# Optimization experiments

Hardware: AMD Instinct MI355X
Metric: run time of the kernel (lower is better)

Reference implementation:

```python
import jax, jax.numpy as jnp
import numpy as np

D_MODEL = 1024
NUM_HEADS = 16
DIM_HEAD = 64
B, NQ, NKV = 2, 2048, 2048


def setup_inputs() -> dict:
    key = jax.random.key(0)
    ks = jax.random.split(key, 12)
    inner = NUM_HEADS * DIM_HEAD
    s_in = 1.0 / np.sqrt(D_MODEL)
    s_o = 1.0 / np.sqrt(inner)
    return {
        "Q": jax.random.normal(ks[0], (B, NQ, D_MODEL), jnp.float32),
        "K": jax.random.normal(ks[1], (B, NKV, D_MODEL), jnp.float32),
        "V": jax.random.normal(ks[2], (B, NKV, D_MODEL), jnp.float32),
        "mask": jax.random.randint(ks[3], (B, 1, NQ, NKV), 0, 2, jnp.int32),
        "W_q": jax.random.normal(ks[4], (D_MODEL, inner), jnp.float32) * s_in,
        "b_q": jnp.zeros((inner,), jnp.float32),
        "W_k": jax.random.normal(ks[5], (D_MODEL, inner), jnp.float32) * s_in,
        "b_k": jnp.zeros((inner,), jnp.float32),
        "W_v": jax.random.normal(ks[6], (D_MODEL, inner), jnp.float32) * s_in,
        "b_v": jnp.zeros((inner,), jnp.float32),
        "W_o": jax.random.normal(ks[7], (inner, D_MODEL), jnp.float32) * s_o,
        "b_o": jnp.zeros((D_MODEL,), jnp.float32),
    }


def reference(Q, K, V, mask, W_q, b_q, W_k, b_k, W_v, b_v, W_o, b_o):
    h, d = NUM_HEADS, DIM_HEAD
    # projections: [b, n, h*d] -> [b, h, n, d]
    def split_heads(x):
        b, n, _ = x.shape
        return x.reshape(b, n, h, d).transpose(0, 2, 1, 3)

    q = split_heads(Q @ W_q + b_q)
    k = split_heads(K @ W_k + b_k)
    v = split_heads(V @ W_v + b_v)

    scores = jnp.einsum("bhqd,bhkd->bhqk", q, k) / jnp.sqrt(jnp.float32(d))
    scores = jnp.where(mask == 0, jnp.float32(-1e9), scores)
    probs = jax.nn.softmax(scores, axis=-1)
    out = jnp.einsum("bhqk,bhkd->bhqd", probs, v)
    out = out.transpose(0, 2, 1, 3).reshape(Q.shape[0], Q.shape[1], h * d)
    return out @ W_o + b_o
```

## Files before the change

### kernel.cpp

```cpp
#include <hip/hip_runtime.h>
#include <hip/hip_bf16.h>
#include <stdint.h>

#define DM   1024
#define NH   16
#define DHD  64
#define BB   2
#define NQS  2048
#define NKVS 2048

typedef __attribute__((ext_vector_type(8))) short short8;
typedef __attribute__((ext_vector_type(4))) float f32x4;
typedef __attribute__((ext_vector_type(16))) float f32x16;
typedef __attribute__((ext_vector_type(4))) unsigned short us4;

static __device__ __forceinline__ unsigned short f2bf(float f) {
  union { float f; unsigned u; } v; v.f = f;
  unsigned r = (v.u + 0x7fffu + ((v.u >> 16) & 1u)) >> 16;
  return (unsigned short)r;
}

#define MFMA(a, b, c)   __builtin_amdgcn_mfma_f32_16x16x32_bf16((a), (b), (c), 0, 0, 0)
#define MFMA32(a, b, c) __builtin_amdgcn_mfma_f32_32x32x16_bf16((a), (b), (c), 0, 0, 0)

__global__ __launch_bounds__(256) void wt_kernel(
    const float* __restrict__ Wq, const float* __restrict__ Wk,
    const float* __restrict__ Wv, const float* __restrict__ Wo,
    unsigned short* __restrict__ wt) {
  __shared__ unsigned short Ls[64][68];
  const int z = blockIdx.z;
  const float* W = (z == 0) ? Wq : (z == 1) ? Wk : (z == 2) ? Wv : Wo;
  unsigned short* out = wt + (size_t)z * 1024 * 1024;
  const int r0 = blockIdx.y * 64, c0 = blockIdx.x * 64;
  const int t = threadIdx.x;
#pragma unroll
  for (int i = 0; i < 4; i++) {
    int idx = t + 256 * i;
    int row = idx >> 4, c4 = (idx & 15) * 4;
    float4 v = *(const float4*)(W + (size_t)(r0 + row) * 1024 + c0 + c4);
    Ls[row][c4 + 0] = f2bf(v.x);
    Ls[row][c4 + 1] = f2bf(v.y);
    Ls[row][c4 + 2] = f2bf(v.z);
    Ls[row][c4 + 3] = f2bf(v.w);
  }
  __syncthreads();
#pragma unroll
  for (int i = 0; i < 4; i++) {
    int idx = t + 256 * i;
    int jj = idx >> 4, k4 = (idx & 15) * 4;
    us4 o;
    o[0] = Ls[k4 + 0][jj];
    o[1] = Ls[k4 + 1][jj];
    o[2] = Ls[k4 + 2][jj];
    o[3] = Ls[k4 + 3][jj];
    *(us4*)(out + (size_t)(c0 + jj) * 1024 + r0 + k4) = o;
  }
}

__global__ __launch_bounds__(256) void maskpack_kernel(
    const int* __restrict__ mask, unsigned long long* __restrict__ pk) {
  const long long total = (long long)BB * NQS * NKVS;
  const long long stride = (long long)gridDim.x * 256;
  for (long long i = (long long)blockIdx.x * 256 + threadIdx.x; i < total; i += stride) {
    int m = mask[i];
    unsigned long long b = __ballot(m != 0);
    if ((i & 63) == 0) pk[i >> 6] = b;
  }
}

__global__ __launch_bounds__(256) void proj_kernel(
    const float* __restrict__ Qin, const float* __restrict__ Kin, const float* __restrict__ Vin,
    const unsigned short* __restrict__ wt,
    const float* __restrict__ bq, const float* __restrict__ bk, const float* __restrict__ bv,
    unsigned short* __restrict__ q_ws, unsigned short* __restrict__ k_ws,
    unsigned short* __restrict__ v_ws) {
  __shared__ unsigned short As[128 * 72];
  __shared__ unsigned short Bs[128 * 72];
  const int z = blockIdx.z;
  const float* X = (z == 0) ? Qin : (z == 1) ? Kin : Vin;
  const float* bias = (z == 0) ? bq : (z == 1) ? bk : bv;
  const unsigned short* Wt = wt + (size_t)z * 1024 * 1024;
  const int m0 = blockIdx.y * 128, j0 = blockIdx.x * 128;
  const int t = threadIdx.x, wid = t >> 6, lane = t & 63, lr = lane & 15, lg = lane >> 4;
  const int wm = wid >> 1, wn = wid & 1;

  f32x4 acc[4][4] = {};
  for (int kt = 0; kt < 16; kt++) {
    const int k0 = kt * 64;
#pragma unroll
    for (int i = 0; i < 8; i++) {
      int idx = t + 256 * i;
      int row = idx >> 4, c4 = (idx & 15) * 4;
      float4 v = *(const float4*)(X + (size_t)(m0 + row) * 1024 + k0 + c4);
      us4 o;
      o[0] = f2bf(v.x); o[1] = f2bf(v.y); o[2] = f2bf(v.z); o[3] = f2bf(v.w);
      *(us4*)(&As[row * 72 + c4]) = o;
    }
#pragma unroll
    for (int i = 0; i < 4; i++) {
      int idx = t + 256 * i;
      int j = idx >> 3, c8 = (idx & 7) * 8;
      short8 v = *(const short8*)(Wt + (size_t)(j0 + j) * 1024 + k0 + c8);
      *(short8*)(&Bs[j * 72 + c8]) = v;
    }
    __syncthreads();
    short8 a[2][4], b[2][4];
#pragma unroll
    for (int ks = 0; ks < 2; ks++)
#pragma unroll
      for (int mf = 0; mf < 4; mf++)
        a[ks][mf] = *(const short8*)(&As[(wm * 64 + mf * 16 + lr) * 72 + ks * 32 + lg * 8]);
#pragma unroll
    for (int ks = 0; ks < 2; ks++)
#pragma unroll
      for (int nf = 0; nf < 4; nf++)
        b[ks][nf] = *(const short8*)(&Bs[(wn * 64 + nf * 16 + lr) * 72 + ks * 32 + lg * 8]);
#pragma unroll
    for (int ks = 0; ks < 2; ks++)
#pragma unroll
      for (int mf = 0; mf < 4; mf++)
#pragma unroll
        for (int nf = 0; nf < 4; nf++)
          acc[mf][nf] = MFMA(a[ks][mf], b[ks][nf], acc[mf][nf]);
    __syncthreads();
  }
#pragma unroll
  for (int nf = 0; nf < 4; nf++) {
    const int j = j0 + wn * 64 + nf * 16 + lr;
    const float bj = bias[j];
    const int h = j >> 6, dd = j & 63;
#pragma unroll
    for (int mf = 0; mf < 4; mf++) {
      const int mb = m0 + wm * 64 + mf * 16 + lg * 4;
      const int b_ = mb >> 11, nb = mb & 2047;
      if (z == 2) {
        us4 o;
#pragma unroll
        for (int r = 0; r < 4; r++) o[r] = f2bf(acc[mf][nf][r] + bj);
        *(us4*)(v_ws + ((size_t)(b_ * NH + h) * DHD + dd) * NKVS + nb) = o;
      } else {
        unsigned short* dst = (z == 0) ? q_ws : k_ws;
        const float sc = (z == 0) ? 0.125f : 1.0f;
#pragma unroll
        for (int r = 0; r < 4; r++) {
          float val = (acc[mf][nf][r] + bj) * sc;
          dst[((size_t)(b_ * NH + h) * NQS + nb + r) * DHD + dd] = f2bf(val);
        }
      }
    }
  }
}

__global__ __launch_bounds__(256) void attn_kernel(
    const unsigned short* __restrict__ q_ws, const unsigned short* __restrict__ k_ws,
    const unsigned short* __restrict__ v_ws, const unsigned long long* __restrict__ pk,
    unsigned short* __restrict__ o_ws) {
  __shared__ float Ml[2][64][2];
  __shared__ float Ol[2][64][36];
  const int h = blockIdx.y, b = blockIdx.z;
  const int bh = b * NH + h;
  const int t = threadIdx.x, wid = t >> 6, lane = t & 63;
  const int l31 = lane & 31, hi = lane >> 5;
  const int qsub = wid & 1, kvh = wid >> 1;
  const int q = blockIdx.x * 64 + qsub * 32 + l31;

  short8 qb[4];
  {
    const unsigned short* qp = q_ws + ((size_t)bh * NQS + q) * DHD + hi * 8;
#pragma unroll
    for (int ks = 0; ks < 4; ks++) qb[ks] = *(const short8*)(qp + ks * 16);
  }
  const unsigned long long* mp = pk + ((size_t)b * NQS + q) * 32;
  const unsigned short* kbase = k_ws + (size_t)bh * NQS * DHD;
  const unsigned short* vbase = v_ws + (size_t)bh * DHD * NKVS;

  f32x16 O[2] = {};
  float m = -1e30f, l = 0.f;

  for (int it = 0; it < 16; it++) {
    const unsigned long long mw = mp[kvh * 16 + it];
#pragma unroll
    for (int st = 0; st < 2; st++) {
      const int kv0 = kvh * 1024 + it * 64 + st * 32;
      const unsigned mword = st ? (unsigned)(mw >> 32) : (unsigned)mw;
      f32x16 S = {};
      {
        const unsigned short* kp = kbase + (size_t)(kv0 + l31) * DHD + hi * 8;
#pragma unroll
        for (int ks = 0; ks < 4; ks++)
          S = MFMA32(*(const short8*)(kp + ks * 16), qb[ks], S);
      }
      float p[16];
      float pmax = -1e30f;
#pragma unroll
      for (int r = 0; r < 16; r++) {
        const int kvr = (r & 3) + 8 * (r >> 2) + 4 * hi;
        const bool bit = (mword >> kvr) & 1u;
        const float sv = bit ? S[r] : -1e30f;
        p[r] = sv;
        pmax = fmaxf(pmax, sv);
      }
      pmax = fmaxf(pmax, __shfl_xor(pmax, 32));
      if (!__all(pmax - m <= 8.f)) {
        const float mn = fmaxf(m, pmax);
        const float sc = __expf(m - mn);
        m = mn; l *= sc;
#pragma unroll
        for (int dt = 0; dt < 2; dt++)
#pragma unroll
          for (int r = 0; r < 16; r++) O[dt][r] *= sc;
      }
      float rs = 0.f;
#pragma unroll
      for (int r = 0; r < 16; r++) {
        p[r] = (p[r] > -1e29f) ? __expf(p[r] - m) : 0.f;
        rs += p[r];
      }
      rs += __shfl_xor(rs, 32);
      l += rs;
      unsigned pk8[8], sw[8];
#pragma unroll
      for (int i = 0; i < 8; i++)
        pk8[i] = (unsigned)f2bf(p[2 * i]) | ((unsigned)f2bf(p[2 * i + 1]) << 16);
#pragma unroll
      for (int i = 0; i < 8; i++) sw[i] = __shfl_xor(pk8[i], 32);
      union { unsigned u[4]; short8 s; } pb0, pb1;
      pb0.u[0] = hi ? sw[2] : pk8[0];
      pb0.u[1] = hi ? sw[3] : pk8[1];
      pb0.u[2] = hi ? pk8[2] : sw[0];
      pb0.u[3] = hi ? pk8[3] : sw[1];
      pb1.u[0] = hi ? sw[6] : pk8[4];
      pb1.u[1] = hi ? sw[7] : pk8[5];
      pb1.u[2] = hi ? pk8[6] : sw[4];
      pb1.u[3] = hi ? pk8[7] : sw[5];
#pragma unroll
      for (int dt = 0; dt < 2; dt++) {
        const unsigned short* vp = vbase + (size_t)(dt * 32 + l31) * NKVS + kv0 + hi * 8;
        short8 va0 = *(const short8*)(vp);
        short8 va1 = *(const short8*)(vp + 16);
        O[dt] = MFMA32(va0, pb0.s, O[dt]);
        O[dt] = MFMA32(va1, pb1.s, O[dt]);
      }
    }
  }
  if (kvh == 1) {
    Ml[qsub][lane][0] = m;
    Ml[qsub][lane][1] = l;
#pragma unroll
    for (int dt = 0; dt < 2; dt++)
#pragma unroll
      for (int g = 0; g < 4; g++) {
        f32x4 v;
#pragma unroll
        for (int j = 0; j < 4; j++) v[j] = O[dt][g * 4 + j];
        *(f32x4*)&Ol[qsub][lane][dt * 16 + g * 4] = v;
      }
  }
  __syncthreads();
  if (kvh == 0) {
    const float m1 = Ml[qsub][lane][0], l1 = Ml[qsub][lane][1];
    const float M = fmaxf(m, m1);
    const float a0 = __expf(m - M), a1 = __expf(m1 - M);
    const float L = l * a0 + l1 * a1;
    const float rinv = (L > 0.f) ? 1.f / L : 0.f;
    const float s0 = a0 * rinv, s1 = a1 * rinv;
#pragma unroll
    for (int dt = 0; dt < 2; dt++)
#pragma unroll
      for (int g = 0; g < 4; g++) {
        us4 o;
#pragma unroll
        for (int j = 0; j < 4; j++) {
          const float v = O[dt][g * 4 + j] * s0 + Ol[qsub][lane][dt * 16 + g * 4 + j] * s1;
          o[j] = f2bf(v);
        }
        const int d = dt * 32 + g * 8 + hi * 4;
        *(us4*)(o_ws + ((size_t)b * NQS + q) * DM + h * DHD + d) = o;
      }
  }
}

__global__ __launch_bounds__(256) void outproj_kernel(
    const unsigned short* __restrict__ Ain, const unsigned short* __restrict__ Wt,
    const float* __restrict__ bo, float* __restrict__ out) {
  __shared__ unsigned short As[128 * 72];
  __shared__ unsigned short Bs[128 * 72];
  const int m0 = blockIdx.y * 128, j0 = blockIdx.x * 128;
  const int t = threadIdx.x, wid = t >> 6, lane = t & 63, lr = lane & 15, lg = lane >> 4;
  const int wm = wid >> 1, wn = wid & 1;

  f32x4 acc[4][4] = {};
  for (int kt = 0; kt < 16; kt++) {
    const int k0 = kt * 64;
#pragma unroll
    for (int i = 0; i < 4; i++) {
      int idx = t + 256 * i;
      int row = idx >> 3, c8 = (idx & 7) * 8;
      *(short8*)(&As[row * 72 + c8]) =
          *(const short8*)(Ain + (size_t)(m0 + row) * 1024 + k0 + c8);
    }
#pragma unroll
    for (int i = 0; i < 4; i++) {
      int idx = t + 256 * i;
      int j = idx >> 3, c8 = (idx & 7) * 8;
      *(short8*)(&Bs[j * 72 + c8]) =
          *(const short8*)(Wt + (size_t)(j0 + j) * 1024 + k0 + c8);
    }
    __syncthreads();
    short8 a[2][4], b[2][4];
#pragma unroll
    for (int ks = 0; ks < 2; ks++)
#pragma unroll
      for (int mf = 0; mf < 4; mf++)
        a[ks][mf] = *(const short8*)(&As[(wm * 64 + mf * 16 + lr) * 72 + ks * 32 + lg * 8]);
#pragma unroll
    for (int ks = 0; ks < 2; ks++)
#pragma unroll
      for (int nf = 0; nf < 4; nf++)
        b[ks][nf] = *(const short8*)(&Bs[(wn * 64 + nf * 16 + lr) * 72 + ks * 32 + lg * 8]);
#pragma unroll
    for (int ks = 0; ks < 2; ks++)
#pragma unroll
      for (int mf = 0; mf < 4; mf++)
#pragma unroll
        for (int nf = 0; nf < 4; nf++)
          acc[mf][nf] = MFMA(a[ks][mf], b[ks][nf], acc[mf][nf]);
    __syncthreads();
  }
#pragma unroll
  for (int nf = 0; nf < 4; nf++) {
    const int j = j0 + wn * 64 + nf * 16 + lr;
    const float bj = bo[j];
#pragma unroll
    for (int mf = 0; mf < 4; mf++) {
      const int mb = m0 + wm * 64 + mf * 16 + lg * 4;
#pragma unroll
      for (int r = 0; r < 4; r++)
        out[(size_t)(mb + r) * 1024 + j] = acc[mf][nf][r] + bj;
    }
  }
}

extern "C" void kernel_launch(void* const* d_in, const int* in_sizes, int n_in,
                              void* d_out, int out_size, void* d_ws, size_t ws_size,
                              hipStream_t stream) {
  (void)in_sizes; (void)n_in; (void)out_size; (void)ws_size;
  const float* Q  = (const float*)d_in[0];
  const float* K  = (const float*)d_in[1];
  const float* V  = (const float*)d_in[2];
  const int* mask = (const int*)d_in[3];
  const float* Wq = (const float*)d_in[4];
  const float* bq = (const float*)d_in[5];
  const float* Wk = (const float*)d_in[6];
  const float* bk = (const float*)d_in[7];
  const float* Wv = (const float*)d_in[8];
  const float* bv = (const float*)d_in[9];
  const float* Wo = (const float*)d_in[10];
  const float* bo = (const float*)d_in[11];
  float* out = (float*)d_out;

  char* ws = (char*)d_ws;
  const size_t SZ_BHND = (size_t)BB * NH * NQS * DHD * 2;
  unsigned short* q_ws = (unsigned short*)(ws);
  unsigned short* k_ws = (unsigned short*)(ws + SZ_BHND);
  unsigned short* v_ws = (unsigned short*)(ws + 2 * SZ_BHND);
  unsigned short* o_ws = (unsigned short*)(ws + 3 * SZ_BHND);
  unsigned short* wt   = (unsigned short*)(ws + 4 * SZ_BHND);
  unsigned long long* pk = (unsigned long long*)(ws + 5 * SZ_BHND);

  hipLaunchKernelGGL(wt_kernel, dim3(16, 16, 4), dim3(256), 0, stream, Wq, Wk, Wv, Wo, wt);
  hipLaunchKernelGGL(maskpack_kernel, dim3(4096), dim3(256), 0, stream, mask, pk);
  hipLaunchKernelGGL(proj_kernel, dim3(8, 32, 3), dim3(256), 0, stream,
                     Q, K, V, wt, bq, bk, bv, q_ws, k_ws, v_ws);
  hipLaunchKernelGGL(attn_kernel, dim3(32, 16, 2), dim3(256), 0, stream,
                     q_ws, k_ws, v_ws, pk, o_ws);
  hipLaunchKernelGGL(outproj_kernel, dim3(8, 32), dim3(256), 0, stream,
                     o_ws, wt + (size_t)3 * 1024 * 1024, bo, out);
}
```

Before: 399.7 us.

## Split attention KV range across four waves per 32-query block

The attention kernel now gives each block 32 queries instead of 64, and its four waves each process a quarter of the KV sequence (512 keys) instead of two query halves times two KV halves. The four partial softmax states are then merged through shared memory by wave 0, and the grid doubles to 2048 blocks. The aim is more blocks for better occupancy and load balance, and shorter per-wave loops. The cost is more K/V traffic per query, since each block rereads all of K/V for only 32 queries, plus a larger reduction step.

```diff
diff --git a/kernel.cpp b/kernel.cpp
--- a/kernel.cpp
+++ b/kernel.cpp
@@ -153,16 +153,15 @@
 
 __global__ __launch_bounds__(256) void attn_kernel(
     const unsigned short* __restrict__ q_ws, const unsigned short* __restrict__ k_ws,
-    const unsigned short* __restrict__ v_ws, const unsigned long long* __restrict__ pk,
+    const unsigned short* __restrict__ v_ws, const unsigned* __restrict__ pk32,
     unsigned short* __restrict__ o_ws) {
-  __shared__ float Ml[2][64][2];
-  __shared__ float Ol[2][64][36];
+  __shared__ float Ol[3][64][34];
+  __shared__ float Ml[3][64][2];
   const int h = blockIdx.y, b = blockIdx.z;
   const int bh = b * NH + h;
-  const int t = threadIdx.x, wid = t >> 6, lane = t & 63;
+  const int t = threadIdx.x, w = t >> 6, lane = t & 63;
   const int l31 = lane & 31, hi = lane >> 5;
-  const int qsub = wid & 1, kvh = wid >> 1;
-  const int q = blockIdx.x * 64 + qsub * 32 + l31;
+  const int q = blockIdx.x * 32 + l31;
 
   short8 qb[4];
   {
@@ -170,82 +169,78 @@
 #pragma unroll
     for (int ks = 0; ks < 4; ks++) qb[ks] = *(const short8*)(qp + ks * 16);
   }
-  const unsigned long long* mp = pk + ((size_t)b * NQS + q) * 32;
-  const unsigned short* kbase = k_ws + (size_t)bh * NQS * DHD;
+  const unsigned* mp = pk32 + ((size_t)b * NQS + q) * 64 + w * 16;
+  const unsigned short* kbase = k_ws + ((size_t)bh * NQS + w * 512) * DHD;
   const unsigned short* vbase = v_ws + (size_t)bh * DHD * NKVS;
 
   f32x16 O[2] = {};
   float m = -1e30f, l = 0.f;
 
   for (int it = 0; it < 16; it++) {
-    const unsigned long long mw = mp[kvh * 16 + it];
-#pragma unroll
-    for (int st = 0; st < 2; st++) {
-      const int kv0 = kvh * 1024 + it * 64 + st * 32;
-      const unsigned mword = st ? (unsigned)(mw >> 32) : (unsigned)mw;
-      f32x16 S = {};
-      {
-        const unsigned short* kp = kbase + (size_t)(kv0 + l31) * DHD + hi * 8;
-#pragma unroll
-        for (int ks = 0; ks < 4; ks++)
-          S = MFMA32(*(const short8*)(kp + ks * 16), qb[ks], S);
-      }
-      float p[16];
-      float pmax = -1e30f;
-#pragma unroll
-      for (int r = 0; r < 16; r++) {
-        const int kvr = (r & 3) + 8 * (r >> 2) + 4 * hi;
-        const bool bit = (mword >> kvr) & 1u;
-        const float sv = bit ? S[r] : -1e30f;
-        p[r] = sv;
-        pmax = fmaxf(pmax, sv);
-      }
-      pmax = fmaxf(pmax, __shfl_xor(pmax, 32));
-      if (!__all(pmax - m <= 8.f)) {
-        const float mn = fmaxf(m, pmax);
-        const float sc = __expf(m - mn);
-        m = mn; l *= sc;
-#pragma unroll
-        for (int dt = 0; dt < 2; dt++)
-#pragma unroll
-          for (int r = 0; r < 16; r++) O[dt][r] *= sc;
-      }
-      float rs = 0.f;
-#pragma unroll
-      for (int r = 0; r < 16; r++) {
-        p[r] = (p[r] > -1e29f) ? __expf(p[r] - m) : 0.f;
-        rs += p[r];
-      }
-      rs += __shfl_xor(rs, 32);
-      l += rs;
-      unsigned pk8[8], sw[8];
-#pragma unroll
-      for (int i = 0; i < 8; i++)
-        pk8[i] = (unsigned)f2bf(p[2 * i]) | ((unsigned)f2bf(p[2 * i + 1]) << 16);
-#pragma unroll
-      for (int i = 0; i < 8; i++) sw[i] = __shfl_xor(pk8[i], 32);
-      union { unsigned u[4]; short8 s; } pb0, pb1;
-      pb0.u[0] = hi ? sw[2] : pk8[0];
-      pb0.u[1] = hi ? sw[3] : pk8[1];
-      pb0.u[2] = hi ? pk8[2] : sw[0];
-      pb0.u[3] = hi ? pk8[3] : sw[1];
-      pb1.u[0] = hi ? sw[6] : pk8[4];
-      pb1.u[1] = hi ? sw[7] : pk8[5];
-      pb1.u[2] = hi ? pk8[6] : sw[4];
-      pb1.u[3] = hi ? pk8[7] : sw[5];
-#pragma unroll
-      for (int dt = 0; dt < 2; dt++) {
-        const unsigned short* vp = vbase + (size_t)(dt * 32 + l31) * NKVS + kv0 + hi * 8;
-        short8 va0 = *(const short8*)(vp);
-        short8 va1 = *(const short8*)(vp + 16);
-        O[dt] = MFMA32(va0, pb0.s, O[dt]);
-        O[dt] = MFMA32(va1, pb1.s, O[dt]);
-      }
-    }
-  }
-  if (kvh == 1) {
-    Ml[qsub][lane][0] = m;
-    Ml[qsub][lane][1] = l;
+    const int kv0 = w * 512 + it * 32;
+    const unsigned mword = mp[it];
+    f32x16 S = {};
+    {
+      const unsigned short* kp = kbase + (size_t)(it * 32 + l31) * DHD + hi * 8;
+#pragma unroll
+      for (int ks = 0; ks < 4; ks++)
+        S = MFMA32(*(const short8*)(kp + ks * 16), qb[ks], S);
+    }
+    float p[16];
+    float pmax = -1e30f;
+#pragma unroll
+    for (int r = 0; r < 16; r++) {
+      const int kvr = (r & 3) + 8 * (r >> 2) + 4 * hi;
+      const bool bit = (mword >> kvr) & 1u;
+      const float sv = bit ? S[r] : -1e30f;
+      p[r] = sv;
+      pmax = fmaxf(pmax, sv);
+    }
+    pmax = fmaxf(pmax, __shfl_xor(pmax, 32));
+    if (!__all(pmax - m <= 8.f)) {
+      const float mn = fmaxf(m, pmax);
+      const float sc = __expf(m - mn);
+      m = mn; l *= sc;
+#pragma unroll
+      for (int dt = 0; dt < 2; dt++)
+#pragma unroll
+        for (int r = 0; r < 16; r++) O[dt][r] *= sc;
+    }
+    float rs = 0.f;
+#pragma unroll
+    for (int r = 0; r < 16; r++) {
+      p[r] = (p[r] > -1e29f) ? __expf(p[r] - m) : 0.f;
+      rs += p[r];
+    }
+    rs += __shfl_xor(rs, 32);
+    l += rs;
+    unsigned pk8[8], sw[8];
+#pragma unroll
+    for (int i = 0; i < 8; i++)
+      pk8[i] = (unsigned)f2bf(p[2 * i]) | ((unsigned)f2bf(p[2 * i + 1]) << 16);
+#pragma unroll
+    for (int i = 0; i < 8; i++) sw[i] = __shfl_xor(pk8[i], 32);
+    union { unsigned u[4]; short8 s; } pb0, pb1;
+    pb0.u[0] = hi ? sw[2] : pk8[0];
+    pb0.u[1] = hi ? sw[3] : pk8[1];
+    pb0.u[2] = hi ? pk8[2] : sw[0];
+    pb0.u[3] = hi ? pk8[3] : sw[1];
+    pb1.u[0] = hi ? sw[6] : pk8[4];
+    pb1.u[1] = hi ? sw[7] : pk8[5];
+    pb1.u[2] = hi ? pk8[6] : sw[4];
+    pb1.u[3] = hi ? pk8[7] : sw[5];
+#pragma unroll
+    for (int dt = 0; dt < 2; dt++) {
+      const unsigned short* vp = vbase + (size_t)(dt * 32 + l31) * NKVS + kv0 + hi * 8;
+      short8 va0 = *(const short8*)(vp);
+      short8 va1 = *(const short8*)(vp + 16);
+      O[dt] = MFMA32(va0, pb0.s, O[dt]);
+      O[dt] = MFMA32(va1, pb1.s, O[dt]);
+    }
+  }
+  if (w) {
+    Ml[w - 1][lane][0] = m;
+    Ml[w - 1][lane][1] = l;
 #pragma unroll
     for (int dt = 0; dt < 2; dt++)
 #pragma unroll
@@ -253,27 +248,46 @@
         f32x4 v;
 #pragma unroll
         for (int j = 0; j < 4; j++) v[j] = O[dt][g * 4 + j];
-        *(f32x4*)&Ol[qsub][lane][dt * 16 + g * 4] = v;
+        *(f32x4*)&Ol[w - 1][lane][dt * 16 + g * 4] = v;
       }
   }
   __syncthreads();
-  if (kvh == 0) {
-    const float m1 = Ml[qsub][lane][0], l1 = Ml[qsub][lane][1];
-    const float M = fmaxf(m, m1);
-    const float a0 = __expf(m - M), a1 = __expf(m1 - M);
-    const float L = l * a0 + l1 * a1;
+  if (w == 0) {
+    float mo[3], lo[3];
+    float M = m;
+#pragma unroll
+    for (int j = 0; j < 3; j++) {
+      mo[j] = Ml[j][lane][0];
+      lo[j] = Ml[j][lane][1];
+      M = fmaxf(M, mo[j]);
+    }
+    const float a0 = __expf(m - M);
+    float aj[3];
+    float L = l * a0;
+#pragma unroll
+    for (int j = 0; j < 3; j++) {
+      aj[j] = __expf(mo[j] - M);
+      L += lo[j] * aj[j];
+    }
     const float rinv = (L > 0.f) ? 1.f / L : 0.f;
-    const float s0 = a0 * rinv, s1 = a1 * rinv;
+    const float s0 = a0 * rinv;
 #pragma unroll
     for (int dt = 0; dt < 2; dt++)
 #pragma unroll
       for (int g = 0; g < 4; g++) {
+        f32x4 acc;
+#pragma unroll
+        for (int j = 0; j < 4; j++) acc[j] = O[dt][g * 4 + j] * s0;
+#pragma unroll
+        for (int j = 0; j < 3; j++) {
+          const f32x4 ov = *(const f32x4*)&Ol[j][lane][dt * 16 + g * 4];
+          const float sj = aj[j] * rinv;
+#pragma unroll
+          for (int jj = 0; jj < 4; jj++) acc[jj] += ov[jj] * sj;
+        }
         us4 o;
 #pragma unroll
-        for (int j = 0; j < 4; j++) {
-          const float v = O[dt][g * 4 + j] * s0 + Ol[qsub][lane][dt * 16 + g * 4 + j] * s1;
-          o[j] = f2bf(v);
-        }
+        for (int jj = 0; jj < 4; jj++) o[jj] = f2bf(acc[jj]);
         const int d = dt * 32 + g * 8 + hi * 4;
         *(us4*)(o_ws + ((size_t)b * NQS + q) * DM + h * DHD + d) = o;
       }
@@ -372,8 +386,8 @@
   hipLaunchKernelGGL(maskpack_kernel, dim3(4096), dim3(256), 0, stream, mask, pk);
   hipLaunchKernelGGL(proj_kernel, dim3(8, 32, 3), dim3(256), 0, stream,
                      Q, K, V, wt, bq, bk, bv, q_ws, k_ws, v_ws);
-  hipLaunchKernelGGL(attn_kernel, dim3(32, 16, 2), dim3(256), 0, stream,
-                     q_ws, k_ws, v_ws, pk, o_ws);
+  hipLaunchKernelGGL(attn_kernel, dim3(64, 16, 2), dim3(256), 0, stream,
+                     q_ws, k_ws, v_ws, (const unsigned*)pk, o_ws);
   hipLaunchKernelGGL(outproj_kernel, dim3(8, 32), dim3(256), 0, stream,
                      o_ws, wt + (size_t)3 * 1024 * 1024, bo, out);
 }
```

New measurement: 385.6 us. -3.5%, faster.
